# Kernel tuning notes

Measured on AMD Instinct MI355X. Metric: run time of the kernel, lower is better.

## Reference

```python
import jax, jax.numpy as jnp
import numpy as np

EMBED = 256
MAX_NL = 2
NP = 9
NH = 1


def bilinear_sample(img, grid):
    # img: [C, H, W]; grid: [N, 2] (x, y) in [-1, 1]
    # F.grid_sample(mode='bilinear', padding_mode='zeros', align_corners=False)
    C, H, W = img.shape
    x = (grid[:, 0] + 1.0) * (W * 0.5) - 0.5
    y = (grid[:, 1] + 1.0) * (H * 0.5) - 0.5
    x0 = jnp.floor(x)
    y0 = jnp.floor(y)
    wx1 = x - x0
    wy1 = y - y0
    img_f = img.reshape(C, H * W)

    def corner(xi, yi, w):
        valid = (xi >= 0) & (xi <= W - 1) & (yi >= 0) & (yi <= H - 1)
        idx = (jnp.clip(yi, 0, H - 1).astype(jnp.int32) * W
               + jnp.clip(xi, 0, W - 1).astype(jnp.int32))
        return img_f[:, idx] * (w * valid)[None, :]

    return (corner(x0, y0, (1 - wx1) * (1 - wy1))
            + corner(x0 + 1, y0, wx1 * (1 - wy1))
            + corner(x0, y0 + 1, (1 - wx1) * wy1)
            + corner(x0 + 1, y0 + 1, wx1 * wy1))  # [C, N]


def setup_inputs() -> dict:
    k = jax.random.key(0)
    ks = jax.random.split(k, 5)
    nq = 20000
    H = W = 128
    nv = H * W
    nl = 2
    C = EMBED
    query = jax.random.normal(ks[0], (1, nq, C), jnp.float32)
    key = jnp.zeros((1, nq, C), jnp.float32)  # unused by forward
    value = jax.random.normal(ks[1], (nl, nv, C), jnp.float32)
    reference_points = jax.random.uniform(ks[2], (1, nq, nl, 2), jnp.float32)
    spatial_shapes = jnp.array([[H, W], [H, W]], jnp.int32)
    W_off = jax.random.normal(ks[3], (C, MAX_NL * NH * NP * 2), jnp.float32) * 0.02
    b_off = jax.random.normal(ks[4], (MAX_NL * NH * NP * 2,), jnp.float32) * 0.02
    return {"query": query, "key": key, "value": value,
            "reference_points": reference_points, "spatial_shapes": spatial_shapes,
            "W_off": W_off, "b_off": b_off}


def reference(query, key, value, reference_points, spatial_shapes, W_off, b_off):
    nl, nv, C = value.shape
    bs, nq, _ = query.shape
    # sampling offsets: [bs, nq, NH, max_nl, NP, 2], sliced to nl levels
    off = (query @ W_off + b_off).reshape(bs, nq, NH, MAX_NL, NP, 2)[:, :, :, :nl]
    # normalizer stacks (W, H) per level
    norm = jnp.stack([spatial_shapes[:, 1], spatial_shapes[:, 0]], -1).astype(query.dtype)
    loc = reference_points[:, :, None, :, None, :] + off / norm[None, None, None, :, None, :]
    grids = 2.0 * loc - 1.0  # [1, nq, 1, nl, NP, 2]
    sampled = []
    for l in range(nl):
        H = int(spatial_shapes[l, 0]); W = int(spatial_shapes[l, 1])
        img = value[l].T.reshape(C, H, W)
        g = grids[0, :, 0, l, :, :].reshape(nq * NP, 2)
        sampled.append(bilinear_sample(img, g).reshape(C, nq, NP))
    # stack levels then flatten points: [1, nq, nl*NP, C]
    kv = jnp.stack(sampled, axis=-2).reshape(C, nq, nl * NP).transpose(1, 2, 0)[None]
    # note: original multiplies by sqrt(dim) (not divide) -- kept faithful
    attn = jax.nn.softmax(jnp.einsum('bqc,bqpc->bqp', query, kv)
                          * jnp.sqrt(jnp.float32(C)), axis=-1)
    return jnp.einsum('bqp,bqpc->bqc', attn, kv)
```

## Files before the change

### kernel.cpp

```cpp
#include <hip/hip_runtime.h>

#define C_EMB 256
#define NPL   9
#define NLV   2
#define NPTS  (NPL * NLV)
#define NJ    (NPTS * 2)

__global__ void transpose_woff(const float* __restrict__ W_off, float* __restrict__ WT) {
    int j = blockIdx.x;
    int c = threadIdx.x;
    WT[j * C_EMB + c] = W_off[c * NJ + j];
}

__device__ __forceinline__ int imin(int a, int b) { return a < b ? a : b; }
__device__ __forceinline__ int imax(int a, int b) { return a > b ? a : b; }

template<int CTRL, int ROW_MASK>
__device__ __forceinline__ float dpp_add(float x) {
    int t = __builtin_amdgcn_update_dpp(0, __builtin_bit_cast(int, x),
                                        CTRL, ROW_MASK, 0xf, true);
    return x + __builtin_bit_cast(float, t);
}

__device__ __forceinline__ float wave_sum_all(float x) {
    x = dpp_add<0x111, 0xf>(x);
    x = dpp_add<0x112, 0xf>(x);
    x = dpp_add<0x114, 0xf>(x);
    x = dpp_add<0x118, 0xf>(x);
    x = dpp_add<0x142, 0xa>(x);
    x = dpp_add<0x143, 0xc>(x);
    int r = __builtin_amdgcn_readlane(__builtin_bit_cast(int, x), 63);
    return __builtin_bit_cast(float, r);
}

template<bool USE_WT>
__global__ __launch_bounds__(128)
void deform_attn_kernel(const float* __restrict__ query,
                        const float* __restrict__ value,
                        const float* __restrict__ refp,
                        const int*   __restrict__ sshapes,
                        const float* __restrict__ WT,
                        const float* __restrict__ W_off,
                        const float* __restrict__ b_off,
                        float*       __restrict__ out,
                        int nq, int nv) {
    const int lane = threadIdx.x & 63;
    const int widx = threadIdx.x >> 6;
    const int q = blockIdx.x * 2 + widx;
    if (q >= nq) return;

    __shared__ int4   s_idx[2][NPTS];
    __shared__ float4 s_w[2][NPTS];

    const int coff = lane * 4;
    const float4 q4 = *reinterpret_cast<const float4*>(query + (size_t)q * C_EMB + coff);

    float ox = 0.f, oy = 0.f;
    #pragma unroll
    for (int j = 0; j < NJ; ++j) {
        float s;
        if (USE_WT) {
            float4 w4 = *reinterpret_cast<const float4*>(WT + j * C_EMB + coff);
            s = q4.x * w4.x + q4.y * w4.y + q4.z * w4.z + q4.w * w4.w;
        } else {
            const float* wp = W_off + (size_t)coff * NJ + j;
            s = q4.x * wp[0] + q4.y * wp[NJ] + q4.z * wp[2 * NJ] + q4.w * wp[3 * NJ];
        }
        s = wave_sum_all(s) + b_off[j];
        if (j == 2 * lane)     ox = s;
        if (j == 2 * lane + 1) oy = s;
    }

    if (lane < NPTS) {
        int l = lane / NPL;
        int Hi = sshapes[l * 2 + 0];
        int Wi = sshapes[l * 2 + 1];
        float fw = (float)Wi, fh = (float)Hi;
        float rx = refp[((size_t)q * NLV + l) * 2 + 0];
        float ry = refp[((size_t)q * NLV + l) * 2 + 1];
        float x = rx * fw + ox - 0.5f;
        float y = ry * fh + oy - 0.5f;
        float x0f = floorf(x), y0f = floorf(y);
        int x0 = (int)x0f, y0 = (int)y0f;
        float wx1 = x - x0f, wy1 = y - y0f;
        float wx0 = 1.f - wx1, wy0 = 1.f - wy1;
        bool vx0 = (x0 >= 0) && (x0 <= Wi - 1);
        bool vx1 = (x0 + 1 >= 0) && (x0 + 1 <= Wi - 1);
        bool vy0 = (y0 >= 0) && (y0 <= Hi - 1);
        bool vy1 = (y0 + 1 >= 0) && (y0 + 1 <= Hi - 1);
        int cx0 = imin(imax(x0, 0), Wi - 1);
        int cx1 = imin(imax(x0 + 1, 0), Wi - 1);
        int cy0 = imin(imax(y0, 0), Hi - 1);
        int cy1 = imin(imax(y0 + 1, 0), Hi - 1);
        int base = l * nv;
        int4 id;
        id.x = base + cy0 * Wi + cx0;
        id.y = base + cy0 * Wi + cx1;
        id.z = base + cy1 * Wi + cx0;
        id.w = base + cy1 * Wi + cx1;
        float4 w;
        w.x = wx0 * wy0 * ((vx0 && vy0) ? 1.f : 0.f);
        w.y = wx1 * wy0 * ((vx1 && vy0) ? 1.f : 0.f);
        w.z = wx0 * wy1 * ((vx0 && vy1) ? 1.f : 0.f);
        w.w = wx1 * wy1 * ((vx1 && vy1) ? 1.f : 0.f);
        s_idx[widx][lane] = id;
        s_w[widx][lane]   = w;
    }
    __builtin_amdgcn_wave_barrier();

    float4 kv[NPTS];
    float  lg[NPTS];
    #pragma unroll
    for (int p = 0; p < NPTS; ++p) {
        int4   id = s_idx[widx][p];
        float4 w  = s_w[widx][p];
        const float4 a = *reinterpret_cast<const float4*>(value + (size_t)id.x * C_EMB + coff);
        const float4 b = *reinterpret_cast<const float4*>(value + (size_t)id.y * C_EMB + coff);
        const float4 c = *reinterpret_cast<const float4*>(value + (size_t)id.z * C_EMB + coff);
        const float4 d = *reinterpret_cast<const float4*>(value + (size_t)id.w * C_EMB + coff);
        float4 acc;
        acc.x = w.x * a.x + w.y * b.x + w.z * c.x + w.w * d.x;
        acc.y = w.x * a.y + w.y * b.y + w.z * c.y + w.w * d.y;
        acc.z = w.x * a.z + w.y * b.z + w.z * c.z + w.w * d.z;
        acc.w = w.x * a.w + w.y * b.w + w.z * c.w + w.w * d.w;
        kv[p] = acc;
        lg[p] = q4.x * acc.x + q4.y * acc.y + q4.z * acc.z + q4.w * acc.w;
    }

    #pragma unroll
    for (int p = 0; p < NPTS; ++p) {
        lg[p] = wave_sum_all(lg[p]) * 16.0f;
    }

    float m = lg[0];
    #pragma unroll
    for (int p = 1; p < NPTS; ++p) m = fmaxf(m, lg[p]);
    float sum = 0.f;
    #pragma unroll
    for (int p = 0; p < NPTS; ++p) { lg[p] = __expf(lg[p] - m); sum += lg[p]; }
    float inv = 1.0f / sum;

    float4 o; o.x = 0.f; o.y = 0.f; o.z = 0.f; o.w = 0.f;
    #pragma unroll
    for (int p = 0; p < NPTS; ++p) {
        o.x += lg[p] * kv[p].x;
        o.y += lg[p] * kv[p].y;
        o.z += lg[p] * kv[p].z;
        o.w += lg[p] * kv[p].w;
    }
    o.x *= inv; o.y *= inv; o.z *= inv; o.w *= inv;
    *reinterpret_cast<float4*>(out + (size_t)q * C_EMB + coff) = o;
}

extern "C" void kernel_launch(void* const* d_in, const int* in_sizes, int n_in,
                              void* d_out, int out_size, void* d_ws, size_t ws_size,
                              hipStream_t stream) {
    const float* query = (const float*)d_in[0];
    const float* value = (const float*)d_in[2];
    const float* refp  = (const float*)d_in[3];
    const int*   ss    = (const int*)d_in[4];
    const float* W_off = (const float*)d_in[5];
    const float* b_off = (const float*)d_in[6];
    float* out = (float*)d_out;

    const int nq = in_sizes[0] / C_EMB;
    const int nl = in_sizes[4] / 2;
    const int nv = in_sizes[2] / (nl * C_EMB);

    const int blocks = (nq + 1) / 2;

    const size_t wt_bytes = (size_t)NJ * C_EMB * sizeof(float);
    if (ws_size >= wt_bytes) {
        float* WT = (float*)d_ws;
        transpose_woff<<<NJ, C_EMB, 0, stream>>>(W_off, WT);
        deform_attn_kernel<true><<<blocks, 128, 0, stream>>>(
            query, value, refp, ss, WT, W_off, b_off, out, nq, nv);
    } else {
        deform_attn_kernel<false><<<blocks, 128, 0, stream>>>(
            query, value, refp, ss, nullptr, W_off, b_off, out, nq, nv);
    }
}
```

Measured before the change: 84.68 us.

## Use online softmax and 32-bit byte offsets to cut register pressure

The kernel now folds each sampled point into a running max, sum and weighted output (online softmax), so it no longer keeps all 18 interpolated vectors and logits live in registers. Value and weight addresses are computed with 32-bit unsigned byte offsets instead of 64-bit size_t arithmetic. A min-blocks-per-CU hint is added to launch bounds. The aim is fewer VGPRs and higher occupancy so more gathers are in flight. The cost is two extra exps and rescaling per point, plus a serial wave reduction per point that may limit how far loads can be overlapped.

New measurement: 90.92 us. 7.4% more time.

```diff
diff --git a/kernel.cpp b/kernel.cpp
--- a/kernel.cpp
+++ b/kernel.cpp
@@ -34,7 +34,7 @@
 }
 
 template<bool USE_WT>
-__global__ __launch_bounds__(128)
+__global__ __launch_bounds__(128, 3)
 void deform_attn_kernel(const float* __restrict__ query,
                         const float* __restrict__ value,
                         const float* __restrict__ refp,
@@ -52,15 +52,17 @@
     __shared__ int4   s_idx[2][NPTS];
     __shared__ float4 s_w[2][NPTS];
 
-    const int coff = lane * 4;
+    const int coff  = lane * 4;
+    const unsigned coff4 = (unsigned)lane * 16u;
     const float4 q4 = *reinterpret_cast<const float4*>(query + (size_t)q * C_EMB + coff);
 
     float ox = 0.f, oy = 0.f;
+    const char* wtb = (const char*)WT;
     #pragma unroll
     for (int j = 0; j < NJ; ++j) {
         float s;
         if (USE_WT) {
-            float4 w4 = *reinterpret_cast<const float4*>(WT + j * C_EMB + coff);
+            float4 w4 = *reinterpret_cast<const float4*>(wtb + ((unsigned)(j * 1024) + coff4));
             s = q4.x * w4.x + q4.y * w4.y + q4.z * w4.z + q4.w * w4.w;
         } else {
             const float* wp = W_off + (size_t)coff * NJ + j;
@@ -108,46 +110,35 @@
     }
     __builtin_amdgcn_wave_barrier();
 
-    float4 kv[NPTS];
-    float  lg[NPTS];
+    const char* vb = (const char*)value;
+    float m = -3.0e38f, ssum = 0.f;
+    float4 o; o.x = 0.f; o.y = 0.f; o.z = 0.f; o.w = 0.f;
     #pragma unroll
     for (int p = 0; p < NPTS; ++p) {
         int4   id = s_idx[widx][p];
         float4 w  = s_w[widx][p];
-        const float4 a = *reinterpret_cast<const float4*>(value + (size_t)id.x * C_EMB + coff);
-        const float4 b = *reinterpret_cast<const float4*>(value + (size_t)id.y * C_EMB + coff);
-        const float4 c = *reinterpret_cast<const float4*>(value + (size_t)id.z * C_EMB + coff);
-        const float4 d = *reinterpret_cast<const float4*>(value + (size_t)id.w * C_EMB + coff);
-        float4 acc;
-        acc.x = w.x * a.x + w.y * b.x + w.z * c.x + w.w * d.x;
-        acc.y = w.x * a.y + w.y * b.y + w.z * c.y + w.w * d.y;
-        acc.z = w.x * a.z + w.y * b.z + w.z * c.z + w.w * d.z;
-        acc.w = w.x * a.w + w.y * b.w + w.z * c.w + w.w * d.w;
-        kv[p] = acc;
-        lg[p] = q4.x * acc.x + q4.y * acc.y + q4.z * acc.z + q4.w * acc.w;
+        const float4 a = *reinterpret_cast<const float4*>(vb + (((unsigned)id.x << 10) + coff4));
+        const float4 b = *reinterpret_cast<const float4*>(vb + (((unsigned)id.y << 10) + coff4));
+        const float4 c = *reinterpret_cast<const float4*>(vb + (((unsigned)id.z << 10) + coff4));
+        const float4 d = *reinterpret_cast<const float4*>(vb + (((unsigned)id.w << 10) + coff4));
+        float4 kvp;
+        kvp.x = w.x * a.x + w.y * b.x + w.z * c.x + w.w * d.x;
+        kvp.y = w.x * a.y + w.y * b.y + w.z * c.y + w.w * d.y;
+        kvp.z = w.x * a.z + w.y * b.z + w.z * c.z + w.w * d.z;
+        kvp.w = w.x * a.w + w.y * b.w + w.z * c.w + w.w * d.w;
+        float dp = q4.x * kvp.x + q4.y * kvp.y + q4.z * kvp.z + q4.w * kvp.w;
+        float lg = wave_sum_all(dp) * 16.0f;
+        float mn = fmaxf(m, lg);
+        float sc = __expf(m - mn);
+        float pv = __expf(lg - mn);
+        ssum = ssum * sc + pv;
+        o.x = o.x * sc + pv * kvp.x;
+        o.y = o.y * sc + pv * kvp.y;
+        o.z = o.z * sc + pv * kvp.z;
+        o.w = o.w * sc + pv * kvp.w;
+        m = mn;
     }
-
-    #pragma unroll
-    for (int p = 0; p < NPTS; ++p) {
-        lg[p] = wave_sum_all(lg[p]) * 16.0f;
-    }
-
-    float m = lg[0];
-    #pragma unroll
-    for (int p = 1; p < NPTS; ++p) m = fmaxf(m, lg[p]);
-    float sum = 0.f;
-    #pragma unroll
-    for (int p = 0; p < NPTS; ++p) { lg[p] = __expf(lg[p] - m); sum += lg[p]; }
-    float inv = 1.0f / sum;
-
-    float4 o; o.x = 0.f; o.y = 0.f; o.z = 0.f; o.w = 0.f;
-    #pragma unroll
-    for (int p = 0; p < NPTS; ++p) {
-        o.x += lg[p] * kv[p].x;
-        o.y += lg[p] * kv[p].y;
-        o.z += lg[p] * kv[p].z;
-        o.w += lg[p] * kv[p].w;
-    }
+    float inv = 1.0f / ssum;
     o.x *= inv; o.y *= inv; o.z *= inv; o.w *= inv;
     *reinterpret_cast<float4*>(out + (size_t)q * C_EMB + coff) = o;
 }
```
